# Kernel optimization log

Hardware: AMD Instinct MI355X
Metric: run time of the kernel (lower is better)

Reference implementation:

```python
import jax, jax.numpy as jnp
import numpy as np


def setup_inputs() -> dict:
    key = jax.random.key(0)
    kq, kk, kv = jax.random.split(key, 3)
    B, H, T, D = 2, 8, 8192, 64
    return {
        "Q": jax.random.normal(kq, (B, H, T, D), dtype=jnp.float32),
        "K": jax.random.normal(kk, (B, H, T, D), dtype=jnp.float32),
        "V": jax.random.normal(kv, (B, H, T, D), dtype=jnp.float32),
        "window_size": 512,
    }


def _gather_bands(x, nb, Wn):
    # x: [B,H,T,D] -> [B,H,nb,3*Wn,D], key blocks (i-1, i, i+1) per query block i
    B, H, T, D = x.shape
    xb = x.reshape(B, H, nb, Wn, D)
    xp = jnp.pad(xb, ((0, 0), (0, 0), (1, 1), (0, 0), (0, 0)))
    return jnp.concatenate([xp[:, :, i:i + nb] for i in range(3)], axis=3)


def reference(Q, K, V, window_size):
    # Sliding-window attention: softmax over keys with |q_idx - kv_idx| <= window_size,
    # computed block-sparsely (only the 3 neighboring key blocks per query block).
    B, H, T, D = Q.shape
    Wn = int(window_size)
    assert T % Wn == 0
    nb = T // Wn
    scale = 1.0 / (D ** 0.5)

    Qb = Q.reshape(B, H, nb, Wn, D)
    Kw = _gather_bands(K, nb, Wn)  # [B,H,nb,3W,D]
    Vw = _gather_bands(V, nb, Wn)

    # scores within the band: [B,H,nb,W,3W]
    s = jnp.einsum('bhnqd,bhnkd->bhnqk', Qb, Kw) * scale

    # exact band mask: global q = n*W + q_loc, global kv = (n-1)*W + k_loc
    q_loc = jnp.arange(Wn)[:, None]
    k_loc = jnp.arange(3 * Wn)[None, :]
    band = jnp.abs(q_loc + Wn - k_loc) <= Wn          # [W, 3W]
    kv_g = (jnp.arange(nb)[:, None] - 1) * Wn + jnp.arange(3 * Wn)[None, :]  # [nb, 3W]
    valid = (kv_g >= 0) & (kv_g < T)
    mask = band[None, :, :] & valid[:, None, :]        # [nb, W, 3W]

    s = jnp.where(mask[None, None], s, -jnp.inf)
    p = jax.nn.softmax(s, axis=-1)
    o = jnp.einsum('bhnqk,bhnkd->bhnqd', p, Vw)
    return o.reshape(B, H, T, D)
```

## Files before the change

kernel.cpp:

```cpp
#include <hip/hip_runtime.h>
#include <hip/hip_bf16.h>
#include <stdint.h>

typedef __attribute__((ext_vector_type(8))) short bf16x8;
typedef __attribute__((ext_vector_type(4))) short bf16x4;
typedef __attribute__((ext_vector_type(4))) float f32x4;

#define T_SEQ   8192
#define D_HEAD  64
#define NHEADS  16
#define WIN     512
#define BQ      256
#define BK      64
#define NTILES  128
#define NQT     32
#define TILE_SH 8192
#define MASKVAL (-1.0e6f)

#define WS_NEEDED ((size_t)NHEADS * NTILES * TILE_SH * sizeof(short))

#define MFMA32(a,b,c) __builtin_amdgcn_mfma_f32_16x16x32_bf16(a,b,c,0,0,0)

__device__ __forceinline__ short f2bf(float f) {
    union { float f; uint32_t u; } v; v.f = f;
    return (short)((v.u + 0x7FFFu + ((v.u >> 16) & 1u)) >> 16);
}

__device__ __forceinline__ uint32_t pkbf2(float lo, float hi) {
    union { __hip_bfloat162 h; uint32_t u; } c;
    c.h = __float22bfloat162_rn(make_float2(lo, hi));
    return c.u;
}

__global__ __launch_bounds__(256, 2)
void prep_kv(const float* __restrict__ Kg, const float* __restrict__ Vg,
             short* __restrict__ KVf)
{
    __shared__ float vt[64 * 65];
    const int tid  = threadIdx.x;
    const int tile = blockIdx.x & (NTILES - 1);
    const int head = blockIdx.x >> 7;
    const size_t off = ((size_t)head * T_SEQ + (size_t)tile * BK) * D_HEAD;
    short* KV = KVf + ((size_t)head * NTILES + tile) * TILE_SH;

    const float* vs = Vg + off;
    #pragma unroll
    for (int i = 0; i < 4; ++i) {
        int idx = tid + 256 * i;
        int row = idx >> 4, c4 = (idx & 15) << 2;
        *(float4*)&vt[row * 65 + c4] = *(const float4*)(vs + row * D_HEAD + c4);
    }

    const float* ksrc = Kg + off;
    #pragma unroll
    for (int i = 0; i < 2; ++i) {
        int b = tid + 256 * i;
        int quad = b & 3, key = (b >> 2) & 15, ks = (b >> 6) & 1, kc = b >> 7;
        const float* src = ksrc + (kc * 16 + key) * D_HEAD + ks * 32 + quad * 8;
        float4 a = *(const float4*)src;
        float4 c = *(const float4*)(src + 4);
        bf16x8 o;
        o[0]=f2bf(a.x); o[1]=f2bf(a.y); o[2]=f2bf(a.z); o[3]=f2bf(a.w);
        o[4]=f2bf(c.x); o[5]=f2bf(c.y); o[6]=f2bf(c.z); o[7]=f2bf(c.w);
        *(bf16x8*)(KV + b * 8) = o;
    }

    __syncthreads();

    #pragma unroll
    for (int i = 0; i < 2; ++i) {
        int b = tid + 256 * i;
        int quad = b & 3, dl = (b >> 2) & 15, nt = (b >> 6) & 3, h = b >> 8;
        int col = nt * 16 + dl;
        bf16x8 o;
        #pragma unroll
        for (int j = 0; j < 4; ++j) o[j]     = f2bf(vt[(h*32 +      quad*4 + j) * 65 + col]);
        #pragma unroll
        for (int j = 0; j < 4; ++j) o[4 + j] = f2bf(vt[(h*32 + 16 + quad*4 + j) * 65 + col]);
        *(bf16x8*)(KV + 4096 + b * 8) = o;
    }
}

__global__ __launch_bounds__(256, 2)
void swa_fwd(const float* __restrict__ Qg, const short* __restrict__ KVf,
             float* __restrict__ Og)
{
    __shared__ __align__(16) short Buf[2][TILE_SH];

    const int tid  = threadIdx.x;
    const int wave = tid >> 6;
    const int lane = tid & 63;
    const int lcol = lane & 15;
    const int quad = lane >> 4;

    const int g    = blockIdx.x;
    const int head = ((g & 7) << 1) | ((g >> 3) & 1);
    const int qt   = g >> 4;
    const int q0   = qt * BQ;
    const int tb   = qt * 4;

    const float* Qp  = Qg  + (size_t)head * T_SEQ * D_HEAD;
    float*       Op  = Og  + (size_t)head * T_SEQ * D_HEAD;
    const short* KVh = KVf + (size_t)head * NTILES * TILE_SH;

    const float qscale = 0.125f * 1.44269504088896340736f;
    const int qrow_w = q0 + wave * 64;

    bf16x8 qf[4][2];
    #pragma unroll
    for (int mt = 0; mt < 4; ++mt) {
        const float* qptr = Qp + (size_t)(qrow_w + mt*16 + lcol) * D_HEAD + quad * 8;
        #pragma unroll
        for (int ks = 0; ks < 2; ++ks) {
            float4 a = *(const float4*)(qptr + ks*32);
            float4 b = *(const float4*)(qptr + ks*32 + 4);
            bf16x8 f;
            f[0]=f2bf(a.x*qscale); f[1]=f2bf(a.y*qscale); f[2]=f2bf(a.z*qscale); f[3]=f2bf(a.w*qscale);
            f[4]=f2bf(b.x*qscale); f[5]=f2bf(b.y*qscale); f[6]=f2bf(b.z*qscale); f[7]=f2bf(b.w*qscale);
            qf[mt][ks] = f;
        }
    }

    f32x4 oacc[4][4];
    float l_run[4];
    const f32x4 zero4 = {0.f, 0.f, 0.f, 0.f};
    #pragma unroll
    for (int mt = 0; mt < 4; ++mt) {
        l_run[mt] = 0.f;
        #pragma unroll
        for (int nt = 0; nt < 4; ++nt) oacc[mt][nt] = zero4;
    }

    int t0 = tb - 8;  if (t0 < 0) t0 = 0;
    int t1 = tb + 11; if (t1 > NTILES - 1) t1 = NTILES - 1;

    {
        const short* src = KVh + (size_t)t0 * TILE_SH + tid * 8;
        #pragma unroll
        for (int i = 0; i < 4; ++i)
            *(bf16x8*)&Buf[0][tid*8 + i*2048] = *(const bf16x8*)(src + i*2048);
    }
    __syncthreads();

    int cur = 0;
    for (int t = t0; t <= t1; ++t) {
        bf16x8 pre[4];
        const bool have = (t < t1);
        if (have) {
            const short* src = KVh + (size_t)(t + 1) * TILE_SH + tid * 8;
            #pragma unroll
            for (int i = 0; i < 4; ++i) pre[i] = *(const bf16x8*)(src + i*2048);
        }

        if (t*BK <= qrow_w + 63 + WIN && t*BK + 63 >= qrow_w - WIN) {
            const short* Kl = Buf[cur];
            const short* Vl = Buf[cur] + 4096;
            const bool edge = (t < tb - 4) || (t > tb + 7);

            #pragma unroll
            for (int h = 0; h < 2; ++h) {
                bf16x4 pq[2][4];
                #pragma unroll
                for (int jj = 0; jj < 2; ++jj) {
                    const int kc = h*2 + jj;
                    bf16x8 kf0 = *(const bf16x8*)&Kl[((kc*2 + 0)*64 + lcol*4 + quad) * 8];
                    bf16x8 kf1 = *(const bf16x8*)&Kl[((kc*2 + 1)*64 + lcol*4 + quad) * 8];
                    f32x4 sc[4];
                    #pragma unroll
                    for (int mt = 0; mt < 4; ++mt) sc[mt] = zero4;
                    #pragma unroll
                    for (int mt = 0; mt < 4; ++mt) {
                        sc[mt] = MFMA32(kf0, qf[mt][0], sc[mt]);
                        sc[mt] = MFMA32(kf1, qf[mt][1], sc[mt]);
                    }
                    if (edge) {
                        const int kg0 = t*BK + kc*16 + quad*4;
                        #pragma unroll
                        for (int mt = 0; mt < 4; ++mt) {
                            const int qg = qrow_w + mt*16 + lcol;
                            #pragma unroll
                            for (int r = 0; r < 4; ++r) {
                                int dq = qg - (kg0 + r);
                                if (dq > WIN || dq < -WIN) sc[mt][r] = MASKVAL;
                            }
                        }
                    }
                    #pragma unroll
                    for (int mt = 0; mt < 4; ++mt) {
                        float p0 = exp2f(sc[mt][0]), p1 = exp2f(sc[mt][1]);
                        float p2 = exp2f(sc[mt][2]), p3 = exp2f(sc[mt][3]);
                        l_run[mt] += (p0 + p1) + (p2 + p3);
                        union { int2 i2; bf16x4 v; } u;
                        u.i2 = make_int2((int)pkbf2(p0, p1), (int)pkbf2(p2, p3));
                        pq[jj][mt] = u.v;
                    }
                }
                bf16x8 pf[4];
                #pragma unroll
                for (int mt = 0; mt < 4; ++mt) {
                    union { bf16x8 v; bf16x4 q[2]; } u;
                    u.q[0] = pq[0][mt]; u.q[1] = pq[1][mt];
                    pf[mt] = u.v;
                }
                #pragma unroll
                for (int nt = 0; nt < 4; ++nt) {
                    bf16x8 vf = *(const bf16x8*)&Vl[((h*4 + nt)*64 + lcol*4 + quad) * 8];
                    #pragma unroll
                    for (int mt = 0; mt < 4; ++mt)
                        oacc[mt][nt] = MFMA32(vf, pf[mt], oacc[mt][nt]);
                }
            }
        }

        if (have) {
            #pragma unroll
            for (int i = 0; i < 4; ++i)
                *(bf16x8*)&Buf[cur ^ 1][tid*8 + i*2048] = pre[i];
        }
        __syncthreads();
        cur ^= 1;
    }

    #pragma unroll
    for (int mt = 0; mt < 4; ++mt) {
        float l = l_run[mt];
        l += __shfl_xor(l, 16, 64);
        l += __shfl_xor(l, 32, 64);
        float inv = 1.0f / l;
        const int qg = qrow_w + mt*16 + lcol;
        float* op = Op + (size_t)qg * D_HEAD + quad*4;
        #pragma unroll
        for (int nt = 0; nt < 4; ++nt) {
            float4 o = { oacc[mt][nt][0]*inv, oacc[mt][nt][1]*inv,
                         oacc[mt][nt][2]*inv, oacc[mt][nt][3]*inv };
            *(float4*)(op + nt*16) = o;
        }
    }
}

#define LDSR    72
#define M_INIT  (-1.0e4f)
__global__ __launch_bounds__(256, 2)
void swa_fwd_fb(const float* __restrict__ Qg, const float* __restrict__ Kg,
                const float* __restrict__ Vg, float* __restrict__ Og)
{
    __shared__ short Ks[BK * LDSR];
    __shared__ short Vs[D_HEAD * LDSR];
    __shared__ short Ps[4 * 32 * LDSR];

    const int tid  = threadIdx.x;
    const int wave = tid >> 6;
    const int lane = tid & 63;
    const int lcol = lane & 15;
    const int quad = lane >> 4;

    const int g    = blockIdx.x;
    const int head = (g >> 3) >> 3;
    const int qt   = ((g & 7) << 3) | ((g >> 3) & 7);
    const int q0   = qt * 128;

    const size_t base = (size_t)head * T_SEQ * D_HEAD;
    const float* Qp = Qg + base;
    const float* Kp = Kg + base;
    const float* Vp = Vg + base;
    float*       Op = Og + base;

    const float qscale = 0.125f * 1.44269504088896340736f;
    const int qrow_w = q0 + wave * 32;

    bf16x8 qf[2][2];
    #pragma unroll
    for (int mt = 0; mt < 2; ++mt) {
        const float* qptr = Qp + (size_t)(qrow_w + mt*16 + lcol) * D_HEAD + quad * 8;
        #pragma unroll
        for (int ks = 0; ks < 2; ++ks) {
            float4 a = *(const float4*)(qptr + ks*32);
            float4 b = *(const float4*)(qptr + ks*32 + 4);
            bf16x8 f;
            f[0]=f2bf(a.x*qscale); f[1]=f2bf(a.y*qscale); f[2]=f2bf(a.z*qscale); f[3]=f2bf(a.w*qscale);
            f[4]=f2bf(b.x*qscale); f[5]=f2bf(b.y*qscale); f[6]=f2bf(b.z*qscale); f[7]=f2bf(b.w*qscale);
            qf[mt][ks] = f;
        }
    }

    f32x4 oacc[2][4];
    float m_run[2][4], l_run[2][4];
    const f32x4 zero4 = {0.f, 0.f, 0.f, 0.f};
    #pragma unroll
    for (int mt = 0; mt < 2; ++mt) {
        #pragma unroll
        for (int r = 0; r < 4; ++r) { m_run[mt][r] = M_INIT; l_run[mt][r] = 0.f; }
        #pragma unroll
        for (int nt = 0; nt < 4; ++nt) oacc[mt][nt] = zero4;
    }

    int t0 = (q0 - WIN) >> 6;            if (t0 < 0) t0 = 0;
    int t1 = (q0 + 127 + WIN) >> 6;      if (t1 > NTILES - 1) t1 = NTILES - 1;

    for (int t = t0; t <= t1; ++t) {
        __syncthreads();
        {
            const float* src = Kp + (size_t)t * BK * D_HEAD;
            #pragma unroll
            for (int i = 0; i < 4; ++i) {
                int f4 = tid + 256*i;
                int row = f4 >> 4, c4 = (f4 & 15) << 2;
                float4 v = *(const float4*)(src + row*D_HEAD + c4);
                short4 hh = { f2bf(v.x), f2bf(v.y), f2bf(v.z), f2bf(v.w) };
                *(short4*)&Ks[row*LDSR + c4] = hh;
            }
            const float* vsrc = Vp + (size_t)t * BK * D_HEAD;
            int col = tid & 63, rb = (tid >> 6) << 2;
            #pragma unroll
            for (int i = 0; i < 4; ++i) {
                int r = rb + 16*i;
                short4 hh = { f2bf(vsrc[(r+0)*D_HEAD + col]),
                              f2bf(vsrc[(r+1)*D_HEAD + col]),
                              f2bf(vsrc[(r+2)*D_HEAD + col]),
                              f2bf(vsrc[(r+3)*D_HEAD + col]) };
                *(short4*)&Vs[col*LDSR + r] = hh;
            }
        }
        __syncthreads();

        f32x4 sc[2][4];
        #pragma unroll
        for (int mt = 0; mt < 2; ++mt)
            #pragma unroll
            for (int kt = 0; kt < 4; ++kt) sc[mt][kt] = zero4;
        #pragma unroll
        for (int kt = 0; kt < 4; ++kt) {
            #pragma unroll
            for (int ks = 0; ks < 2; ++ks) {
                bf16x8 kf = *(const bf16x8*)&Ks[(kt*16 + lcol)*LDSR + ks*32 + quad*8];
                sc[0][kt] = MFMA32(qf[0][ks], kf, sc[0][kt]);
                sc[1][kt] = MFMA32(qf[1][ks], kf, sc[1][kt]);
            }
        }

        const int kb = t * BK + lcol;
        #pragma unroll
        for (int mt = 0; mt < 2; ++mt) {
            const int qrow = qrow_w + mt*16 + quad*4;
            #pragma unroll
            for (int kt = 0; kt < 4; ++kt) {
                int kg = kb + kt*16;
                #pragma unroll
                for (int r = 0; r < 4; ++r) {
                    int dq = (qrow + r) - kg;
                    if (dq > WIN || dq < -WIN) sc[mt][kt][r] = MASKVAL;
                }
            }
            float tm[4], al[4], rs[4];
            #pragma unroll
            for (int r = 0; r < 4; ++r)
                tm[r] = fmaxf(fmaxf(sc[mt][0][r], sc[mt][1][r]), fmaxf(sc[mt][2][r], sc[mt][3][r]));
            #pragma unroll
            for (int off = 1; off < 16; off <<= 1)
                #pragma unroll
                for (int r = 0; r < 4; ++r)
                    tm[r] = fmaxf(tm[r], __shfl_xor(tm[r], off, 64));
            #pragma unroll
            for (int r = 0; r < 4; ++r) {
                float mn = fmaxf(m_run[mt][r], tm[r]);
                al[r] = exp2f(m_run[mt][r] - mn);
                m_run[mt][r] = mn;
                rs[r] = 0.f;
            }
            #pragma unroll
            for (int kt = 0; kt < 4; ++kt)
                #pragma unroll
                for (int r = 0; r < 4; ++r) {
                    float p = exp2f(sc[mt][kt][r] - m_run[mt][r]);
                    sc[mt][kt][r] = p;
                    rs[r] += p;
                }
            #pragma unroll
            for (int off = 1; off < 16; off <<= 1)
                #pragma unroll
                for (int r = 0; r < 4; ++r)
                    rs[r] += __shfl_xor(rs[r], off, 64);
            #pragma unroll
            for (int r = 0; r < 4; ++r)
                l_run[mt][r] = l_run[mt][r]*al[r] + rs[r];
            #pragma unroll
            for (int nt = 0; nt < 4; ++nt)
                #pragma unroll
                for (int r = 0; r < 4; ++r) oacc[mt][nt][r] *= al[r];
            short* pw = &Ps[(wave*32 + mt*16 + quad*4) * LDSR];
            #pragma unroll
            for (int kt = 0; kt < 4; ++kt)
                #pragma unroll
                for (int r = 0; r < 4; ++r)
                    pw[r*LDSR + kt*16 + lcol] = f2bf(sc[mt][kt][r]);
        }

        const short* pr = &Ps[wave*32*LDSR];
        #pragma unroll
        for (int ks = 0; ks < 2; ++ks) {
            bf16x8 pf0 = *(const bf16x8*)&pr[(lcol     )*LDSR + ks*32 + quad*8];
            bf16x8 pf1 = *(const bf16x8*)&pr[(16 + lcol)*LDSR + ks*32 + quad*8];
            #pragma unroll
            for (int nt = 0; nt < 4; ++nt) {
                bf16x8 vf = *(const bf16x8*)&Vs[(nt*16 + lcol)*LDSR + ks*32 + quad*8];
                oacc[0][nt] = MFMA32(pf0, vf, oacc[0][nt]);
                oacc[1][nt] = MFMA32(pf1, vf, oacc[1][nt]);
            }
        }
    }

    #pragma unroll
    for (int mt = 0; mt < 2; ++mt)
        #pragma unroll
        for (int r = 0; r < 4; ++r) {
            int row = qrow_w + mt*16 + quad*4 + r;
            float inv = 1.0f / l_run[mt][r];
            float* op = Op + (size_t)row * D_HEAD + lcol;
            #pragma unroll
            for (int nt = 0; nt < 4; ++nt)
                op[nt*16] = oacc[mt][nt][r] * inv;
        }
}

extern "C" void kernel_launch(void* const* d_in, const int* in_sizes, int n_in,
                              void* d_out, int out_size, void* d_ws, size_t ws_size,
                              hipStream_t stream)
{
    const float* Q = (const float*)d_in[0];
    const float* K = (const float*)d_in[1];
    const float* V = (const float*)d_in[2];
    float* O = (float*)d_out;

    if (ws_size >= WS_NEEDED) {
        short* KVf = (short*)d_ws;
        prep_kv<<<dim3(NHEADS * NTILES), dim3(256), 0, stream>>>(K, V, KVf);
        swa_fwd<<<dim3(NHEADS * NQT), dim3(256), 0, stream>>>(Q, KVf, O);
    } else {
        swa_fwd_fb<<<dim3(NHEADS * 64), dim3(256), 0, stream>>>(Q, K, V, O);
    }
}
```

Before: 205.5 us.

## Drop LDS staging, load K/V fragments directly from global with smaller query tiles

The main attention kernel no longer double-buffers K/V tiles through shared memory with block-wide barriers. Each wave now reads its K and V MFMA fragments straight from the pre-packed global workspace. Query tiles shrink from 256 to 128 rows (32 per wave), which doubles the grid, and occupancy is raised to 4 blocks per CU. Each wave walks only its own tight key-tile range and masks only the boundary tiles. This removes LDS traffic and synchronisation, but K/V are now fetched redundantly by every wave and lean on L2/L1 caching.

```diff
diff --git a/kernel.cpp b/kernel.cpp
--- a/kernel.cpp
+++ b/kernel.cpp
@@ -10,10 +10,8 @@
 #define D_HEAD  64
 #define NHEADS  16
 #define WIN     512
-#define BQ      256
 #define BK      64
 #define NTILES  128
-#define NQT     32
 #define TILE_SH 8192
 #define MASKVAL (-1.0e6f)
 
@@ -81,12 +79,10 @@
     }
 }
 
-__global__ __launch_bounds__(256, 2)
+__global__ __launch_bounds__(256, 4)
 void swa_fwd(const float* __restrict__ Qg, const short* __restrict__ KVf,
              float* __restrict__ Og)
 {
-    __shared__ __align__(16) short Buf[2][TILE_SH];
-
     const int tid  = threadIdx.x;
     const int wave = tid >> 6;
     const int lane = tid & 63;
@@ -94,22 +90,21 @@
     const int quad = lane >> 4;
 
     const int g    = blockIdx.x;
-    const int head = ((g & 7) << 1) | ((g >> 3) & 1);
-    const int qt   = g >> 4;
-    const int q0   = qt * BQ;
-    const int tb   = qt * 4;
+    const int head = g >> 6;
+    const int qt   = ((g & 7) << 3) | ((g >> 3) & 7);
+    const int q0   = qt * 128;
 
     const float* Qp  = Qg  + (size_t)head * T_SEQ * D_HEAD;
     float*       Op  = Og  + (size_t)head * T_SEQ * D_HEAD;
     const short* KVh = KVf + (size_t)head * NTILES * TILE_SH;
 
     const float qscale = 0.125f * 1.44269504088896340736f;
-    const int qrow_w = q0 + wave * 64;
-
-    bf16x8 qf[4][2];
-    #pragma unroll
-    for (int mt = 0; mt < 4; ++mt) {
-        const float* qptr = Qp + (size_t)(qrow_w + mt*16 + lcol) * D_HEAD + quad * 8;
+    const int qw = q0 + wave * 32;
+
+    bf16x8 qf[2][2];
+    #pragma unroll
+    for (int mt = 0; mt < 2; ++mt) {
+        const float* qptr = Qp + (size_t)(qw + mt*16 + lcol) * D_HEAD + quad * 8;
         #pragma unroll
         for (int ks = 0; ks < 2; ++ks) {
             float4 a = *(const float4*)(qptr + ks*32);
@@ -121,113 +116,100 @@
         }
     }
 
-    f32x4 oacc[4][4];
-    float l_run[4];
+    f32x4 oacc[2][4];
+    float lr[2] = {0.f, 0.f};
     const f32x4 zero4 = {0.f, 0.f, 0.f, 0.f};
     #pragma unroll
-    for (int mt = 0; mt < 4; ++mt) {
-        l_run[mt] = 0.f;
+    for (int mt = 0; mt < 2; ++mt)
         #pragma unroll
         for (int nt = 0; nt < 4; ++nt) oacc[mt][nt] = zero4;
-    }
-
-    int t0 = tb - 8;  if (t0 < 0) t0 = 0;
-    int t1 = tb + 11; if (t1 > NTILES - 1) t1 = NTILES - 1;
-
-    {
-        const short* src = KVh + (size_t)t0 * TILE_SH + tid * 8;
-        #pragma unroll
-        for (int i = 0; i < 4; ++i)
-            *(bf16x8*)&Buf[0][tid*8 + i*2048] = *(const bf16x8*)(src + i*2048);
-    }
-    __syncthreads();
-
-    int cur = 0;
+
+    int t0 = (qw - WIN) >> 6;           if (t0 < 0) t0 = 0;
+    int t1 = (qw + 31 + WIN) >> 6;      if (t1 > NTILES - 1) t1 = NTILES - 1;
+
+    const int koff = (lcol * 4 + quad) * 8;
+
     for (int t = t0; t <= t1; ++t) {
-        bf16x8 pre[4];
-        const bool have = (t < t1);
-        if (have) {
-            const short* src = KVh + (size_t)(t + 1) * TILE_SH + tid * 8;
-            #pragma unroll
-            for (int i = 0; i < 4; ++i) pre[i] = *(const bf16x8*)(src + i*2048);
-        }
-
-        if (t*BK <= qrow_w + 63 + WIN && t*BK + 63 >= qrow_w - WIN) {
-            const short* Kl = Buf[cur];
-            const short* Vl = Buf[cur] + 4096;
-            const bool edge = (t < tb - 4) || (t > tb + 7);
-
-            #pragma unroll
-            for (int h = 0; h < 2; ++h) {
-                bf16x4 pq[2][4];
-                #pragma unroll
-                for (int jj = 0; jj < 2; ++jj) {
-                    const int kc = h*2 + jj;
-                    bf16x8 kf0 = *(const bf16x8*)&Kl[((kc*2 + 0)*64 + lcol*4 + quad) * 8];
-                    bf16x8 kf1 = *(const bf16x8*)&Kl[((kc*2 + 1)*64 + lcol*4 + quad) * 8];
-                    f32x4 sc[4];
+        const short* KT = KVh + (size_t)t * TILE_SH;
+
+        bf16x8 kf[8];
+        #pragma unroll
+        for (int i = 0; i < 8; ++i)
+            kf[i] = *(const bf16x8*)(KT + i * 512 + koff);
+
+        f32x4 sc[4][2];
+        #pragma unroll
+        for (int kc = 0; kc < 4; ++kc) { sc[kc][0] = zero4; sc[kc][1] = zero4; }
+        #pragma unroll
+        for (int kc = 0; kc < 4; ++kc)
+            #pragma unroll
+            for (int mt = 0; mt < 2; ++mt) {
+                sc[kc][mt] = MFMA32(kf[kc*2    ], qf[mt][0], sc[kc][mt]);
+                sc[kc][mt] = MFMA32(kf[kc*2 + 1], qf[mt][1], sc[kc][mt]);
+            }
+
+        bf16x8 vf[8];
+        #pragma unroll
+        for (int i = 0; i < 8; ++i)
+            vf[i] = *(const bf16x8*)(KT + 4096 + i * 512 + koff);
+
+        const bool full = (t*BK >= qw + 31 - WIN) && (t*BK + 63 <= qw + WIN);
+        if (!full) {
+            #pragma unroll
+            for (int kc = 0; kc < 4; ++kc) {
+                const int kg0 = t*BK + kc*16 + quad*4;
+                #pragma unroll
+                for (int mt = 0; mt < 2; ++mt) {
+                    const int qg = qw + mt*16 + lcol;
                     #pragma unroll
-                    for (int mt = 0; mt < 4; ++mt) sc[mt] = zero4;
-                    #pragma unroll
-                    for (int mt = 0; mt < 4; ++mt) {
-                        sc[mt] = MFMA32(kf0, qf[mt][0], sc[mt]);
-                        sc[mt] = MFMA32(kf1, qf[mt][1], sc[mt]);
-                    }
-                    if (edge) {
-                        const int kg0 = t*BK + kc*16 + quad*4;
-                        #pragma unroll
-                        for (int mt = 0; mt < 4; ++mt) {
-                            const int qg = qrow_w + mt*16 + lcol;
-                            #pragma unroll
-                            for (int r = 0; r < 4; ++r) {
-                                int dq = qg - (kg0 + r);
-                                if (dq > WIN || dq < -WIN) sc[mt][r] = MASKVAL;
-                            }
-                        }
-                    }
-                    #pragma unroll
-                    for (int mt = 0; mt < 4; ++mt) {
-                        float p0 = exp2f(sc[mt][0]), p1 = exp2f(sc[mt][1]);
-                        float p2 = exp2f(sc[mt][2]), p3 = exp2f(sc[mt][3]);
-                        l_run[mt] += (p0 + p1) + (p2 + p3);
-                        union { int2 i2; bf16x4 v; } u;
-                        u.i2 = make_int2((int)pkbf2(p0, p1), (int)pkbf2(p2, p3));
-                        pq[jj][mt] = u.v;
+                    for (int r = 0; r < 4; ++r) {
+                        int dq = qg - (kg0 + r);
+                        if (dq > WIN || dq < -WIN) sc[kc][mt][r] = MASKVAL;
                     }
                 }
-                bf16x8 pf[4];
-                #pragma unroll
-                for (int mt = 0; mt < 4; ++mt) {
-                    union { bf16x8 v; bf16x4 q[2]; } u;
-                    u.q[0] = pq[0][mt]; u.q[1] = pq[1][mt];
-                    pf[mt] = u.v;
-                }
-                #pragma unroll
-                for (int nt = 0; nt < 4; ++nt) {
-                    bf16x8 vf = *(const bf16x8*)&Vl[((h*4 + nt)*64 + lcol*4 + quad) * 8];
-                    #pragma unroll
-                    for (int mt = 0; mt < 4; ++mt)
-                        oacc[mt][nt] = MFMA32(vf, pf[mt], oacc[mt][nt]);
-                }
-            }
-        }
-
-        if (have) {
-            #pragma unroll
-            for (int i = 0; i < 4; ++i)
-                *(bf16x8*)&Buf[cur ^ 1][tid*8 + i*2048] = pre[i];
-        }
-        __syncthreads();
-        cur ^= 1;
-    }
-
-    #pragma unroll
-    for (int mt = 0; mt < 4; ++mt) {
-        float l = l_run[mt];
+            }
+        }
+
+        bf16x4 pq[4][2];
+        #pragma unroll
+        for (int kc = 0; kc < 4; ++kc)
+            #pragma unroll
+            for (int mt = 0; mt < 2; ++mt) {
+                float p0 = __builtin_amdgcn_exp2f(sc[kc][mt][0]);
+                float p1 = __builtin_amdgcn_exp2f(sc[kc][mt][1]);
+                float p2 = __builtin_amdgcn_exp2f(sc[kc][mt][2]);
+                float p3 = __builtin_amdgcn_exp2f(sc[kc][mt][3]);
+                lr[mt] += (p0 + p1) + (p2 + p3);
+                union { int2 i2; bf16x4 v; } u;
+                u.i2 = make_int2((int)pkbf2(p0, p1), (int)pkbf2(p2, p3));
+                pq[kc][mt] = u.v;
+            }
+
+        #pragma unroll
+        for (int h = 0; h < 2; ++h) {
+            bf16x8 pf[2];
+            #pragma unroll
+            for (int mt = 0; mt < 2; ++mt) {
+                union { bf16x8 v; bf16x4 q[2]; } u;
+                u.q[0] = pq[h*2][mt]; u.q[1] = pq[h*2 + 1][mt];
+                pf[mt] = u.v;
+            }
+            #pragma unroll
+            for (int nt = 0; nt < 4; ++nt) {
+                bf16x8 v8 = vf[h*4 + nt];
+                oacc[0][nt] = MFMA32(v8, pf[0], oacc[0][nt]);
+                oacc[1][nt] = MFMA32(v8, pf[1], oacc[1][nt]);
+            }
+        }
+    }
+
+    #pragma unroll
+    for (int mt = 0; mt < 2; ++mt) {
+        float l = lr[mt];
         l += __shfl_xor(l, 16, 64);
         l += __shfl_xor(l, 32, 64);
         float inv = 1.0f / l;
-        const int qg = qrow_w + mt*16 + lcol;
+        const int qg = qw + mt*16 + lcol;
         float* op = Op + (size_t)qg * D_HEAD + quad*4;
         #pragma unroll
         for (int nt = 0; nt < 4; ++nt) {
@@ -434,7 +416,7 @@
     if (ws_size >= WS_NEEDED) {
         short* KVf = (short*)d_ws;
         prep_kv<<<dim3(NHEADS * NTILES), dim3(256), 0, stream>>>(K, V, KVf);
-        swa_fwd<<<dim3(NHEADS * NQT), dim3(256), 0, stream>>>(Q, KVf, O);
+        swa_fwd<<<dim3(NHEADS * 64), dim3(256), 0, stream>>>(Q, KVf, O);
     } else {
         swa_fwd_fb<<<dim3(NHEADS * 64), dim3(256), 0, stream>>>(Q, K, V, O);
     }
```

After: 217.1 us. 5.7% more time.
